# Optimization experiments

Measured on AMD Instinct MI355X. Metric: run time of the kernel, lower is better.

The kernel has to match this reference:

```python
import jax, jax.numpy as jnp
import numpy as np

N, B, G, D = 262144, 4096, 8, 7
NODE_DIM, GLOBAL_DIM, HIDDEN = 128, 128, 64
NEG = -1000000000.0


def setup_inputs() -> dict:
    key = jax.random.key(0)
    ks = jax.random.split(key, 7)
    node_features = jax.random.normal(ks[0], (N, NODE_DIM), jnp.float32)
    global_features = jax.random.normal(ks[1], (B, GLOBAL_DIM), jnp.float32)
    group_mask_nodes = jax.random.randint(ks[2], (N,), 0, 2) == 1
    batch = jnp.sort(jax.random.randint(ks[3], (N,), 0, B)).astype(jnp.int32)
    maneuver_mask = jax.random.randint(ks[4], (B, G, D), 0, 2) == 1
    W1 = jax.random.normal(ks[5], (NODE_DIM + GLOBAL_DIM, HIDDEN), jnp.float32) * 0.0625
    b1 = jnp.zeros((HIDDEN,), jnp.float32)
    W2 = jax.random.normal(ks[6], (HIDDEN, D), jnp.float32) * 0.125
    b2 = jnp.zeros((D,), jnp.float32)
    return {"node_features": node_features, "global_features": global_features,
            "group_mask_nodes": group_mask_nodes, "batch": batch,
            "maneuver_mask": maneuver_mask, "W1": W1, "b1": b1, "W2": W2, "b2": b2}


def reference(node_features, global_features, group_mask_nodes, batch, maneuver_mask, W1, b1, W2, b2):
    # Per-batch ragged group index: g_idx[i] = (# selected rows with same batch id before i).
    sel = group_mask_nodes
    sel_i = sel.astype(jnp.int32)
    csum = jnp.cumsum(sel_i)                                   # inclusive cumsum over selected rows
    counts = jax.ops.segment_sum(sel_i, batch, num_segments=B)  # selected rows per batch
    offsets = jnp.concatenate([jnp.zeros(1, jnp.int32), jnp.cumsum(counts)[:-1].astype(jnp.int32)])
    g_idx = csum - 1 - offsets[batch]                          # valid only where sel
    valid = sel & (g_idx < G)

    # Batched tiny MLP: concat(node, global[batch]) @ W1 done as split matmul to avoid materializing concat.
    glob = global_features[batch]                              # [N, GLOBAL_DIM] gather
    h = jax.nn.relu(node_features @ W1[:NODE_DIM] + glob @ W1[NODE_DIM:] + b1)
    out = h @ W2 + b2                                          # [N, D]

    # Scatter into padded [B, G+1, D]; invalid rows routed to dummy group slot G (sliced off).
    logits = jnp.full((B, G + 1, D), NEG, dtype=out.dtype)
    b_s = jnp.where(valid, batch, 0)
    g_s = jnp.where(valid, g_idx, G)
    logits = logits.at[b_s, g_s].set(out)
    logits = logits[:, :G, :]
    logits = jnp.where(maneuver_mask, logits, jnp.float32(NEG))
    return logits.reshape(B, G * D)
```

## Files before the change

kernel.cpp:

```cpp
#include <hip/hip_runtime.h>
#include <hip/hip_bf16.h>

#define G_SLOTS   8
#define D_OUT     7
#define NODE_DIM  128
#define GLOB_DIM  128
#define HIDDEN    64
#define NEG_VAL   (-1000000000.0f)

__global__ void seg_starts_kernel(const int* __restrict__ batch,
                                  int* __restrict__ starts, int N, int B) {
    int i = blockIdx.x * blockDim.x + threadIdx.x;
    if (i >= N) return;
    int b = batch[i];
    if (i == 0) {
        for (int bb = 0; bb <= b; ++bb) starts[bb] = 0;
    } else {
        int pb = batch[i - 1];
        for (int bb = pb + 1; bb <= b; ++bb) starts[bb] = i;
    }
    if (i == N - 1) {
        for (int bb = b + 1; bb <= B; ++bb) starts[bb] = N;
    }
}

__global__ void find_slots_kernel(const int* __restrict__ sel,
                                  const int* __restrict__ starts,
                                  int* __restrict__ slot_node, int B) {
    int wave = (int)((blockIdx.x * blockDim.x + threadIdx.x) >> 6);
    int lane = (int)(threadIdx.x & 63);
    if (wave >= B) return;
    int b = wave;
    int start = starts[b], end = starts[b + 1];

    int found = 0;
    for (int base = start; base < end && found < G_SLOTS; base += 64) {
        int i = base + lane;
        bool s = (i < end) && (sel[i] != 0);
        unsigned long long m = __ballot(s);
        if (s) {
            int rank = found + __popcll(m & ((1ull << lane) - 1ull));
            if (rank < G_SLOTS) slot_node[b * G_SLOTS + rank] = i;
        }
        found += __popcll(m);
    }
    int f = found < G_SLOTS ? found : G_SLOTS;
    if (lane < G_SLOTS - f) slot_node[b * G_SLOTS + f + lane] = -1;
}

__global__ void glob_mlp_kernel(const float* __restrict__ glob,
                                const float* __restrict__ W1,
                                const float* __restrict__ b1,
                                float* __restrict__ gh, int B) {
    __shared__ float w1g[GLOB_DIM * HIDDEN];
    __shared__ float globl[4 * GLOB_DIM];

    int t = threadIdx.x;
    int b0 = blockIdx.x * 4;
#pragma unroll
    for (int it = 0; it < 8; ++it) {
        int idx = it * 256 + t;
        *(float4*)&w1g[idx * 4] = *(const float4*)&W1[NODE_DIM * HIDDEN + idx * 4];
    }
    if (t < 128) {
        *(float4*)&globl[t * 4] = *(const float4*)&glob[(size_t)b0 * GLOB_DIM + t * 4];
    }
    __syncthreads();

    int w = t >> 6, lane = t & 63;
    float acc = b1[lane];
#pragma unroll 8
    for (int k = 0; k < GLOB_DIM; ++k) {
        acc = fmaf(globl[w * GLOB_DIM + k], w1g[k * HIDDEN + lane], acc);
    }
    gh[(size_t)(b0 + w) * HIDDEN + lane] = acc;
}

#define XSTRIDE 129
__global__ __launch_bounds__(256) void node_mlp_kernel(
        const float* __restrict__ node,
        const int* __restrict__ slot_node,
        const int* __restrict__ mmask,
        const float* __restrict__ W1,
        const float* __restrict__ W2,
        const float* __restrict__ b2,
        const float* __restrict__ gh,
        float* __restrict__ out) {
    __shared__ float w1n[NODE_DIM * HIDDEN];
    __shared__ float xlds[64 * XSTRIDE];
    __shared__ float w2l[HIDDEN * D_OUT];
    __shared__ float b2l[D_OUT];
    __shared__ float pout[4 * 64 * D_OUT];
    __shared__ int   nidxl[64];

    int t = threadIdx.x;
    int slot0 = blockIdx.x * 64;

    if (t < 64) nidxl[t] = slot_node[slot0 + t];
#pragma unroll
    for (int it = 0; it < 8; ++it) {
        int idx = it * 256 + t;
        *(float4*)&w1n[idx * 4] = *(const float4*)&W1[idx * 4];
    }
    if (t < 112) {
        *(float4*)&w2l[t * 4] = *(const float4*)&W2[t * 4];
    }
    if (t < D_OUT) b2l[t] = b2[t];
    __syncthreads();

    {
        int r = t >> 2, q = t & 3;
        int nidx = nidxl[r];
        int cbase = q * 32;
        if (nidx >= 0) {
            const float* src = node + (size_t)nidx * NODE_DIM + cbase;
#pragma unroll
            for (int j = 0; j < 8; ++j) {
                float4 v = *(const float4*)&src[j * 4];
                xlds[r * XSTRIDE + cbase + j * 4 + 0] = v.x;
                xlds[r * XSTRIDE + cbase + j * 4 + 1] = v.y;
                xlds[r * XSTRIDE + cbase + j * 4 + 2] = v.z;
                xlds[r * XSTRIDE + cbase + j * 4 + 3] = v.w;
            }
        } else {
#pragma unroll
            for (int j = 0; j < 32; ++j) xlds[r * XSTRIDE + cbase + j] = 0.0f;
        }
    }
    __syncthreads();

    int sl = t & 63, part = t >> 6;
    int slot = slot0 + sl;
    int b = slot >> 3;
    int hbase = part * 16;

    float acc[16];
#pragma unroll
    for (int j = 0; j < 4; ++j) {
        float4 v = *(const float4*)&gh[(size_t)b * HIDDEN + hbase + j * 4];
        acc[j * 4 + 0] = v.x; acc[j * 4 + 1] = v.y;
        acc[j * 4 + 2] = v.z; acc[j * 4 + 3] = v.w;
    }

#pragma unroll 4
    for (int k = 0; k < NODE_DIM; ++k) {
        float xk = xlds[sl * XSTRIDE + k];
        const float* wrow = &w1n[k * HIDDEN + hbase];
#pragma unroll
        for (int hh = 0; hh < 16; ++hh) {
            acc[hh] = fmaf(xk, wrow[hh], acc[hh]);
        }
    }

    float p[D_OUT];
#pragma unroll
    for (int d = 0; d < D_OUT; ++d) p[d] = (part == 0) ? b2l[d] : 0.0f;
#pragma unroll
    for (int hh = 0; hh < 16; ++hh) {
        float h = fmaxf(acc[hh], 0.0f);
        const float* w2row = &w2l[(hbase + hh) * D_OUT];
#pragma unroll
        for (int d = 0; d < D_OUT; ++d) p[d] = fmaf(h, w2row[d], p[d]);
    }
#pragma unroll
    for (int d = 0; d < D_OUT; ++d) pout[part * (64 * D_OUT) + sl * D_OUT + d] = p[d];
    __syncthreads();

    if (t < 64) {
        int nidx = nidxl[t];
        int obase = (slot0 + t) * D_OUT;
#pragma unroll
        for (int d = 0; d < D_OUT; ++d) {
            float v = pout[0 * 448 + t * D_OUT + d] + pout[1 * 448 + t * D_OUT + d]
                    + pout[2 * 448 + t * D_OUT + d] + pout[3 * 448 + t * D_OUT + d];
            bool mk = mmask[obase + d] != 0;
            out[obase + d] = (nidx >= 0 && mk) ? v : NEG_VAL;
        }
    }
}

extern "C" void kernel_launch(void* const* d_in, const int* in_sizes, int n_in,
                              void* d_out, int out_size, void* d_ws, size_t ws_size,
                              hipStream_t stream) {
    const float* node  = (const float*)d_in[0];
    const float* glob  = (const float*)d_in[1];
    const int*   sel   = (const int*)d_in[2];
    const int*   batch = (const int*)d_in[3];
    const int*   mmask = (const int*)d_in[4];
    const float* W1    = (const float*)d_in[5];
    const float* b1    = (const float*)d_in[6];
    const float* W2    = (const float*)d_in[7];
    const float* b2    = (const float*)d_in[8];
    float* out = (float*)d_out;

    int N = in_sizes[3];
    int B = in_sizes[1] / GLOB_DIM;

    int*   slot_node = (int*)d_ws;
    int*   starts    = (int*)((char*)d_ws + (size_t)B * G_SLOTS * 4);
    float* gh        = (float*)((char*)d_ws + (size_t)B * G_SLOTS * 4 + (size_t)(B + 64) * 4);

    seg_starts_kernel<<<(N + 255) / 256, 256, 0, stream>>>(batch, starts, N, B);
    find_slots_kernel<<<(B * 64 + 255) / 256, 256, 0, stream>>>(sel, starts, slot_node, B);
    glob_mlp_kernel<<<B / 4, 256, 0, stream>>>(glob, W1, b1, gh, B);
    node_mlp_kernel<<<(B * G_SLOTS) / 64, 256, 0, stream>>>(
        node, slot_node, mmask, W1, W2, b2, gh, out);
}
```

Baseline: 206.0 us.

## Fuse slot finding, global MLP and node MLP into one kernel

Merges the find_slots, glob_mlp and node_mlp kernels into a single kernel. Each block now handles 8 batches: it computes their global hidden projection into shared memory, finds the selected node slots with wave ballots, then runs the node MLP. This removes two launches and the workspace round trips for slot indices and gh. The node MLP is remapped so four consecutive threads share a slot and combine partial outputs with xor shuffles instead of an LDS reduction, and W1 rows are read as float4. In exchange, each block reads the global W1 half directly from global memory without LDS staging, and the sel scan is serialized ahead of the MLP inside the block.

Result: no change. 204.8 us (-0.6%).

```diff
diff --git a/kernel.cpp b/kernel.cpp
--- a/kernel.cpp
+++ b/kernel.cpp
@@ -7,6 +7,8 @@
 #define GLOB_DIM  128
 #define HIDDEN    64
 #define NEG_VAL   (-1000000000.0f)
+#define XSTRIDE   129
+#define GH_STRIDE 68
 
 __global__ void seg_starts_kernel(const int* __restrict__ batch,
                                   int* __restrict__ starts, int N, int B) {
@@ -24,88 +26,73 @@
     }
 }
 
-__global__ void find_slots_kernel(const int* __restrict__ sel,
-                                  const int* __restrict__ starts,
-                                  int* __restrict__ slot_node, int B) {
-    int wave = (int)((blockIdx.x * blockDim.x + threadIdx.x) >> 6);
-    int lane = (int)(threadIdx.x & 63);
-    if (wave >= B) return;
-    int b = wave;
-    int start = starts[b], end = starts[b + 1];
-
-    int found = 0;
-    for (int base = start; base < end && found < G_SLOTS; base += 64) {
-        int i = base + lane;
-        bool s = (i < end) && (sel[i] != 0);
-        unsigned long long m = __ballot(s);
-        if (s) {
-            int rank = found + __popcll(m & ((1ull << lane) - 1ull));
-            if (rank < G_SLOTS) slot_node[b * G_SLOTS + rank] = i;
-        }
-        found += __popcll(m);
-    }
-    int f = found < G_SLOTS ? found : G_SLOTS;
-    if (lane < G_SLOTS - f) slot_node[b * G_SLOTS + f + lane] = -1;
-}
-
-__global__ void glob_mlp_kernel(const float* __restrict__ glob,
-                                const float* __restrict__ W1,
-                                const float* __restrict__ b1,
-                                float* __restrict__ gh, int B) {
-    __shared__ float w1g[GLOB_DIM * HIDDEN];
-    __shared__ float globl[4 * GLOB_DIM];
+__global__ __launch_bounds__(256) void fused_mlp_kernel(
+        const float* __restrict__ node,
+        const float* __restrict__ glob,
+        const int* __restrict__ sel,
+        const int* __restrict__ starts,
+        const int* __restrict__ mmask,
+        const float* __restrict__ W1,
+        const float* __restrict__ b1,
+        const float* __restrict__ W2,
+        const float* __restrict__ b2,
+        float* __restrict__ out) {
+    __shared__ __align__(16) float w1n[NODE_DIM * HIDDEN];
+    __shared__ __align__(16) float xlds[64 * XSTRIDE];
+    __shared__ __align__(16) float gh_l[G_SLOTS * GH_STRIDE];
+    __shared__ __align__(16) float w2l[HIDDEN * D_OUT];
+    __shared__ __align__(16) float b2l[D_OUT + 1];
+    __shared__ __align__(16) int   starts_l[G_SLOTS + 1];
+    __shared__ __align__(16) int   nidxl[64];
 
     int t = threadIdx.x;
-    int b0 = blockIdx.x * 4;
-#pragma unroll
-    for (int it = 0; it < 8; ++it) {
-        int idx = it * 256 + t;
-        *(float4*)&w1g[idx * 4] = *(const float4*)&W1[NODE_DIM * HIDDEN + idx * 4];
-    }
-    if (t < 128) {
-        *(float4*)&globl[t * 4] = *(const float4*)&glob[(size_t)b0 * GLOB_DIM + t * 4];
-    }
-    __syncthreads();
+    int b0 = (int)blockIdx.x * 8;
+    int slot0 = (int)blockIdx.x * 64;
 
-    int w = t >> 6, lane = t & 63;
-    float acc = b1[lane];
-#pragma unroll 8
-    for (int k = 0; k < GLOB_DIM; ++k) {
-        acc = fmaf(globl[w * GLOB_DIM + k], w1g[k * HIDDEN + lane], acc);
-    }
-    gh[(size_t)(b0 + w) * HIDDEN + lane] = acc;
-}
-
-#define XSTRIDE 129
-__global__ __launch_bounds__(256) void node_mlp_kernel(
-        const float* __restrict__ node,
-        const int* __restrict__ slot_node,
-        const int* __restrict__ mmask,
-        const float* __restrict__ W1,
-        const float* __restrict__ W2,
-        const float* __restrict__ b2,
-        const float* __restrict__ gh,
-        float* __restrict__ out) {
-    __shared__ float w1n[NODE_DIM * HIDDEN];
-    __shared__ float xlds[64 * XSTRIDE];
-    __shared__ float w2l[HIDDEN * D_OUT];
-    __shared__ float b2l[D_OUT];
-    __shared__ float pout[4 * 64 * D_OUT];
-    __shared__ int   nidxl[64];
-
-    int t = threadIdx.x;
-    int slot0 = blockIdx.x * 64;
-
-    if (t < 64) nidxl[t] = slot_node[slot0 + t];
 #pragma unroll
     for (int it = 0; it < 8; ++it) {
         int idx = it * 256 + t;
         *(float4*)&w1n[idx * 4] = *(const float4*)&W1[idx * 4];
     }
-    if (t < 112) {
-        *(float4*)&w2l[t * 4] = *(const float4*)&W2[t * 4];
+    if (t < 112) *(float4*)&w2l[t * 4] = *(const float4*)&W2[t * 4];
+    if (t < D_OUT) b2l[t] = b2[t];
+    if (t < 9) starts_l[t] = starts[b0 + t];
+
+    {
+        int bb = t >> 5;
+        int h0 = (t & 31) * 2;
+        const float* grow = glob + (size_t)(b0 + bb) * GLOB_DIM;
+        float ax = b1[h0], ay = b1[h0 + 1];
+#pragma unroll 8
+        for (int k = 0; k < GLOB_DIM; ++k) {
+            float g = grow[k];
+            ax = fmaf(g, W1[(NODE_DIM + k) * HIDDEN + h0],     ax);
+            ay = fmaf(g, W1[(NODE_DIM + k) * HIDDEN + h0 + 1], ay);
+        }
+        gh_l[bb * GH_STRIDE + h0]     = ax;
+        gh_l[bb * GH_STRIDE + h0 + 1] = ay;
     }
-    if (t < D_OUT) b2l[t] = b2[t];
+    __syncthreads();
+
+    {
+        int w = t >> 6, lane = t & 63;
+        for (int bi = w * 2; bi < w * 2 + 2; ++bi) {
+            int start = starts_l[bi], end = starts_l[bi + 1];
+            int found = 0;
+            for (int base = start; base < end && found < G_SLOTS; base += 64) {
+                int i = base + lane;
+                bool s = (i < end) && (sel[i] != 0);
+                unsigned long long m = __ballot(s);
+                if (s) {
+                    int rank = found + __popcll(m & ((1ull << lane) - 1ull));
+                    if (rank < G_SLOTS) nidxl[bi * G_SLOTS + rank] = i;
+                }
+                found += __popcll(m);
+            }
+            int f = found < G_SLOTS ? found : G_SLOTS;
+            if (lane < G_SLOTS - f) nidxl[bi * G_SLOTS + f + lane] = -1;
+        }
+    }
     __syncthreads();
 
     {
@@ -129,52 +116,55 @@
     }
     __syncthreads();
 
-    int sl = t & 63, part = t >> 6;
-    int slot = slot0 + sl;
-    int b = slot >> 3;
-    int hbase = part * 16;
+    {
+        int sl = t >> 2, part = t & 3;
+        int bl = sl >> 3;
+        int hbase = part * 16;
 
-    float acc[16];
+        float acc[16];
 #pragma unroll
-    for (int j = 0; j < 4; ++j) {
-        float4 v = *(const float4*)&gh[(size_t)b * HIDDEN + hbase + j * 4];
-        acc[j * 4 + 0] = v.x; acc[j * 4 + 1] = v.y;
-        acc[j * 4 + 2] = v.z; acc[j * 4 + 3] = v.w;
-    }
+        for (int j = 0; j < 16; ++j) acc[j] = gh_l[bl * GH_STRIDE + hbase + j];
 
 #pragma unroll 4
-    for (int k = 0; k < NODE_DIM; ++k) {
-        float xk = xlds[sl * XSTRIDE + k];
-        const float* wrow = &w1n[k * HIDDEN + hbase];
+        for (int k = 0; k < NODE_DIM; ++k) {
+            float xk = xlds[sl * XSTRIDE + k];
+            float4 w0  = *(const float4*)&w1n[k * HIDDEN + hbase + 0];
+            float4 w1v = *(const float4*)&w1n[k * HIDDEN + hbase + 4];
+            float4 w2v = *(const float4*)&w1n[k * HIDDEN + hbase + 8];
+            float4 w3v = *(const float4*)&w1n[k * HIDDEN + hbase + 12];
+            acc[0]  = fmaf(xk, w0.x,  acc[0]);  acc[1]  = fmaf(xk, w0.y,  acc[1]);
+            acc[2]  = fmaf(xk, w0.z,  acc[2]);  acc[3]  = fmaf(xk, w0.w,  acc[3]);
+            acc[4]  = fmaf(xk, w1v.x, acc[4]);  acc[5]  = fmaf(xk, w1v.y, acc[5]);
+            acc[6]  = fmaf(xk, w1v.z, acc[6]);  acc[7]  = fmaf(xk, w1v.w, acc[7]);
+            acc[8]  = fmaf(xk, w2v.x, acc[8]);  acc[9]  = fmaf(xk, w2v.y, acc[9]);
+            acc[10] = fmaf(xk, w2v.z, acc[10]); acc[11] = fmaf(xk, w2v.w, acc[11]);
+            acc[12] = fmaf(xk, w3v.x, acc[12]); acc[13] = fmaf(xk, w3v.y, acc[13]);
+            acc[14] = fmaf(xk, w3v.z, acc[14]); acc[15] = fmaf(xk, w3v.w, acc[15]);
+        }
+
+        float p[D_OUT];
+#pragma unroll
+        for (int d = 0; d < D_OUT; ++d) p[d] = (part == 0) ? b2l[d] : 0.0f;
 #pragma unroll
         for (int hh = 0; hh < 16; ++hh) {
-            acc[hh] = fmaf(xk, wrow[hh], acc[hh]);
+            float h = fmaxf(acc[hh], 0.0f);
+            const float* w2row = &w2l[(hbase + hh) * D_OUT];
+#pragma unroll
+            for (int d = 0; d < D_OUT; ++d) p[d] = fmaf(h, w2row[d], p[d]);
         }
-    }
-
-    float p[D_OUT];
-#pragma unroll
-    for (int d = 0; d < D_OUT; ++d) p[d] = (part == 0) ? b2l[d] : 0.0f;
-#pragma unroll
-    for (int hh = 0; hh < 16; ++hh) {
-        float h = fmaxf(acc[hh], 0.0f);
-        const float* w2row = &w2l[(hbase + hh) * D_OUT];
-#pragma unroll
-        for (int d = 0; d < D_OUT; ++d) p[d] = fmaf(h, w2row[d], p[d]);
-    }
-#pragma unroll
-    for (int d = 0; d < D_OUT; ++d) pout[part * (64 * D_OUT) + sl * D_OUT + d] = p[d];
-    __syncthreads();
-
-    if (t < 64) {
-        int nidx = nidxl[t];
-        int obase = (slot0 + t) * D_OUT;
 #pragma unroll
         for (int d = 0; d < D_OUT; ++d) {
-            float v = pout[0 * 448 + t * D_OUT + d] + pout[1 * 448 + t * D_OUT + d]
-                    + pout[2 * 448 + t * D_OUT + d] + pout[3 * 448 + t * D_OUT + d];
-            bool mk = mmask[obase + d] != 0;
-            out[obase + d] = (nidx >= 0 && mk) ? v : NEG_VAL;
+            p[d] += __shfl_xor(p[d], 1);
+            p[d] += __shfl_xor(p[d], 2);
+        }
+        if (part == 0) {
+            int nidx = nidxl[sl];
+            int obase = (slot0 + sl) * D_OUT;
+#pragma unroll
+            for (int d = 0; d < D_OUT; ++d) {
+                bool mk = mmask[obase + d] != 0;
+                out[obase + d] = (nidx >= 0 && mk) ? p[d] : NEG_VAL;
+            }
         }
     }
 }
@@ -196,13 +186,9 @@
     int N = in_sizes[3];
     int B = in_sizes[1] / GLOB_DIM;
 
-    int*   slot_node = (int*)d_ws;
-    int*   starts    = (int*)((char*)d_ws + (size_t)B * G_SLOTS * 4);
-    float* gh        = (float*)((char*)d_ws + (size_t)B * G_SLOTS * 4 + (size_t)(B + 64) * 4);
+    int* starts = (int*)d_ws;
 
     seg_starts_kernel<<<(N + 255) / 256, 256, 0, stream>>>(batch, starts, N, B);
-    find_slots_kernel<<<(B * 64 + 255) / 256, 256, 0, stream>>>(sel, starts, slot_node, B);
-    glob_mlp_kernel<<<B / 4, 256, 0, stream>>>(glob, W1, b1, gh, B);
-    node_mlp_kernel<<<(B * G_SLOTS) / 64, 256, 0, stream>>>(
-        node, slot_node, mmask, W1, W2, b2, gh, out);
+    fused_mlp_kernel<<<(B * G_SLOTS) / 64, 256, 0, stream>>>(
+        node, glob, sel, starts, mmask, W1, b1, W2, b2, out);
 }
```
